# Kernel optimization log

Measured on AMD Instinct MI355X. Metric: run time of the kernel, lower is better.

Reference implementation:

```python
import jax, jax.numpy as jnp
import numpy as np

N = 50000
E = 800000
IN_FEAT = 128
HEADS = 2
HEAD_DIM = 64  # hidden_feat // num_heads for 'concat'
HIDDEN = HEADS * HEAD_DIM
N_CLASSES = 16
NEG_SLOPE = 0.2
BN_EPS = 1e-5


def setup_inputs() -> dict:
    key = jax.random.key(0)
    ks = jax.random.split(key, 20)
    s = 0.1  # weight scale for numerical sanity
    return {
        "x": jax.random.normal(ks[0], (N, IN_FEAT), jnp.float32),
        "src0": jax.random.randint(ks[1], (E,), 0, N, jnp.int32),
        "dst0": jax.random.randint(ks[2], (E,), 0, N, jnp.int32),
        "ew0": jax.random.uniform(ks[3], (E,), jnp.float32),
        "src1": jax.random.randint(ks[4], (E,), 0, N, jnp.int32),
        "dst1": jax.random.randint(ks[5], (E,), 0, N, jnp.int32),
        "ew1": jax.random.uniform(ks[6], (E,), jnp.float32),
        "fc_w0": jax.random.normal(ks[7], (HIDDEN, IN_FEAT), jnp.float32) * s,
        "bias0": jnp.zeros((HIDDEN,), jnp.float32),
        "attn_l0": jax.random.normal(ks[8], (HEADS, HEAD_DIM), jnp.float32) * s,
        "attn_r0": jax.random.normal(ks[9], (HEADS, HEAD_DIM), jnp.float32) * s,
        "fc_w1": jax.random.normal(ks[10], (HIDDEN, IN_FEAT), jnp.float32) * s,
        "bias1": jnp.zeros((HIDDEN,), jnp.float32),
        "attn_l1": jax.random.normal(ks[11], (HEADS, HEAD_DIM), jnp.float32) * s,
        "attn_r1": jax.random.normal(ks[12], (HEADS, HEAD_DIM), jnp.float32) * s,
        "skip_w": jax.random.normal(ks[13], (HIDDEN, IN_FEAT), jnp.float32) * s,
        "skip_b": jnp.zeros((HIDDEN,), jnp.float32),
        "bn_gamma": jnp.ones((HIDDEN,), jnp.float32),
        "bn_beta": jnp.zeros((HIDDEN,), jnp.float32),
        "clf_w": jax.random.normal(ks[14], (N_CLASSES, HIDDEN), jnp.float32) * s,
        "clf_b": jnp.zeros((N_CLASSES,), jnp.float32),
    }


def _weighted_gat(x, src, dst, ew, fc_w, bias, attn_l, attn_r):
    # DGL GATConv with per-edge weight scaling of attention.
    f = (x @ fc_w.T).reshape(N, HEADS, HEAD_DIM)          # [N,H,D]
    el = jnp.sum(f * attn_l, axis=-1)                      # [N,H]
    er = jnp.sum(f * attn_r, axis=-1)                      # [N,H]
    e = jax.nn.leaky_relu(el[src] + er[dst], NEG_SLOPE)    # [E,H]
    # edge softmax over incoming edges of each dst, numerically stable
    m = jax.ops.segment_max(e, dst, num_segments=N)        # [N,H]
    ex = jnp.exp(e - m[dst])
    den = jax.ops.segment_sum(ex, dst, num_segments=N)     # [N,H]
    alpha = ex / den[dst]                                  # [E,H]
    alpha = alpha * ew[:, None]                            # edge-weight scaling
    msg = alpha[..., None] * f[src]                        # [E,H,D]
    out = jax.ops.segment_sum(msg, dst, num_segments=N)    # [N,H,D]
    return out + bias.reshape(1, HEADS, HEAD_DIM)


def reference(x, src0, dst0, ew0, src1, dst1, ew1,
              fc_w0, bias0, attn_l0, attn_r0,
              fc_w1, bias1, attn_l1, attn_r1,
              skip_w, skip_b, bn_gamma, bn_beta, clf_w, clf_b):
    # HeteroGraphConv with aggregate='sum': sum per-relation GAT outputs
    h2 = _weighted_gat(x, src0, dst0, ew0, fc_w0, bias0, attn_l0, attn_r0) \
       + _weighted_gat(x, src1, dst1, ew1, fc_w1, bias1, attn_l1, attn_r1)
    # multihead 'concat' aggregate with relu: flatten heads
    h2 = jax.nn.relu(h2).reshape(N, HIDDEN)
    # linear skip + residual add (dropout is identity at eval)
    h = (x @ skip_w.T + skip_b) + h2
    # classifier: BatchNorm1d (batch stats) -> ReLU -> Linear
    mu = jnp.mean(h, axis=0)
    var = jnp.mean((h - mu) ** 2, axis=0)
    hn = (h - mu) * jax.lax.rsqrt(var + BN_EPS) * bn_gamma + bn_beta
    logits = jax.nn.relu(hn) @ clf_w.T + clf_b
    return logits
```

## Files before the change

kernel.cpp:

```cpp
#include <hip/hip_runtime.h>
#include <hip/hip_bf16.h>

#define N_NODES 50000
#define N_EDGES 800000
#define HID 128
#define NEG_SLOPE 0.2f
#define BN_EPS 1e-5f

#define NBLK 256
#define BINSZ 512
#define BINSH 9
#define NBINS 98

typedef __bf16 v8bf __attribute__((ext_vector_type(8)));
typedef float v4f __attribute__((ext_vector_type(4)));

__device__ __forceinline__ float leaky(float v) {
    return (v > 0.f) ? v : v * NEG_SLOPE;
}
__device__ __forceinline__ unsigned int f2bu(float f) {
    __hip_bfloat16 b = __float2bfloat16(f);
    return (unsigned int)*reinterpret_cast<unsigned short*>(&b);
}
__device__ __forceinline__ unsigned int pack2bf(float lo, float hi) {
    return f2bu(lo) | (f2bu(hi) << 16);
}

__global__ __launch_bounds__(256) void k_bincount(const int* __restrict__ dst0,
                                                  const int* __restrict__ dst1,
                                                  int* __restrict__ bincnt) {
    int rel = blockIdx.y;
    const int* dst = rel ? dst1 : dst0;
    __shared__ int cnt[NBINS];
    for (int i = threadIdx.x; i < NBINS; i += 256) cnt[i] = 0;
    __syncthreads();
    const int CH = (N_EDGES + NBLK - 1) / NBLK;
    int b0 = blockIdx.x * CH;
    int b1 = min(N_EDGES, b0 + CH);
    for (int e = b0 + threadIdx.x; e < b1; e += 256)
        atomicAdd(&cnt[dst[e] >> BINSH], 1);
    __syncthreads();
    for (int i = threadIdx.x; i < NBINS; i += 256)
        bincnt[rel * NBINS * NBLK + i * NBLK + blockIdx.x] = cnt[i];
}

__global__ __launch_bounds__(1024) void k_binscan(int* __restrict__ bincnt) {
    int* a = bincnt + blockIdx.x * NBINS * NBLK;
    const int TOT = NBINS * NBLK;
    const int CH = (TOT + 1023) / 1024;
    int tid = threadIdx.x;
    int base = tid * CH;
    int lv[CH];
    int sum = 0;
    for (int i = 0; i < CH; i++) {
        int idx = base + i;
        int v = (idx < TOT) ? a[idx] : 0;
        lv[i] = sum;
        sum += v;
    }
    __shared__ int ls[1024];
    ls[tid] = sum;
    __syncthreads();
    for (int ofs = 1; ofs < 1024; ofs <<= 1) {
        int v = (tid >= ofs) ? ls[tid - ofs] : 0;
        __syncthreads();
        ls[tid] += v;
        __syncthreads();
    }
    int pre = tid ? ls[tid - 1] : 0;
    for (int i = 0; i < CH; i++) {
        int idx = base + i;
        if (idx < TOT) a[idx] = pre + lv[i];
    }
}

__global__ __launch_bounds__(256) void k_binscatter(const int* __restrict__ dst0,
                                                    const int* __restrict__ dst1,
                                                    const int* __restrict__ src0,
                                                    const int* __restrict__ src1,
                                                    const float* __restrict__ ew0,
                                                    const float* __restrict__ ew1,
                                                    const int* __restrict__ bincnt,
                                                    int2* __restrict__ pairs0,
                                                    int2* __restrict__ pairs1) {
    int rel = blockIdx.y;
    const int* dst = rel ? dst1 : dst0;
    const int* src = rel ? src1 : src0;
    const float* ew = rel ? ew1 : ew0;
    int2* pairs = rel ? pairs1 : pairs0;
    __shared__ int cur[NBINS];
    for (int i = threadIdx.x; i < NBINS; i += 256)
        cur[i] = bincnt[rel * NBINS * NBLK + i * NBLK + blockIdx.x];
    __syncthreads();
    const int CH = (N_EDGES + NBLK - 1) / NBLK;
    int b0 = blockIdx.x * CH;
    int b1 = min(N_EDGES, b0 + CH);
    for (int e = b0 + threadIdx.x; e < b1; e += 256) {
        int d = dst[e];
        int pos = atomicAdd(&cur[d >> BINSH], 1);
        unsigned int packed = (unsigned int)(d & (BINSZ - 1)) |
                              ((unsigned int)src[e] << BINSH);
        pairs[pos] = make_int2((int)packed, __float_as_int(ew[e]));
    }
}

__global__ __launch_bounds__(256) void k_csr(const int* __restrict__ bincnt,
                                             const int2* __restrict__ pairs0,
                                             const int2* __restrict__ pairs1,
                                             const float* __restrict__ el0,
                                             const float* __restrict__ el1,
                                             int* __restrict__ offs0,
                                             int* __restrict__ offs1,
                                             int4* __restrict__ rec0,
                                             int4* __restrict__ rec1) {
    int rel = blockIdx.y;
    const int2* pairs = rel ? pairs1 : pairs0;
    const float* el = rel ? el1 : el0;
    int* offs = rel ? offs1 : offs0;
    int4* rec = rel ? rec1 : rec0;
    int bin = blockIdx.x;
    int tid = threadIdx.x;
    const int* bc = bincnt + rel * NBINS * NBLK;
    int pbase = bc[bin * NBLK];
    int pend = (bin < NBINS - 1) ? bc[(bin + 1) * NBLK] : N_EDGES;
    int n0 = bin << BINSH;
    int nn = min(N_NODES - n0, BINSZ);

    __shared__ int s_deg[BINSZ];
    __shared__ int s_ts[256];
    for (int i = tid; i < BINSZ; i += 256) s_deg[i] = 0;
    __syncthreads();
    for (int p = pbase + tid; p < pend; p += 256)
        atomicAdd(&s_deg[((unsigned int)pairs[p].x) & (BINSZ - 1)], 1);
    __syncthreads();

    int d0 = s_deg[tid * 2], d1 = s_deg[tid * 2 + 1];
    s_ts[tid] = d0 + d1;
    __syncthreads();
    for (int ofs = 1; ofs < 256; ofs <<= 1) {
        int v = (tid >= ofs) ? s_ts[tid - ofs] : 0;
        __syncthreads();
        s_ts[tid] += v;
        __syncthreads();
    }
    int pre = tid ? s_ts[tid - 1] : 0;
    s_deg[tid * 2] = pbase + pre;
    s_deg[tid * 2 + 1] = pbase + pre + d0;
    __syncthreads();

    for (int l = tid; l < nn; l += 256) offs[n0 + l] = s_deg[l];
    if (bin == NBINS - 1 && tid == 0) offs[N_NODES] = N_EDGES;
    __syncthreads();

    for (int p = pbase + tid; p < pend; p += 256) {
        int2 pr = pairs[p];
        unsigned int u = (unsigned int)pr.x;
        int dl = (int)(u & (BINSZ - 1));
        int s = (int)(u >> BINSH);
        int pos = atomicAdd(&s_deg[dl], 1);
        float2 ev = *(const float2*)(el + 2 * s);
        rec[pos] = make_int4(s, pr.y,
                             __float_as_int(ev.x), __float_as_int(ev.y));
    }
}

__global__ __launch_bounds__(256) void k_gemm_mfma(
    const float* __restrict__ x,
    const float* __restrict__ w0, const float* __restrict__ w1,
    const float* __restrict__ wsk, const float* __restrict__ skip_b,
    const float* __restrict__ al0, const float* __restrict__ ar0,
    const float* __restrict__ al1, const float* __restrict__ ar1,
    unsigned short* __restrict__ fb0, unsigned short* __restrict__ fb1,
    float* __restrict__ el0, float* __restrict__ er0,
    float* __restrict__ el1, float* __restrict__ er1,
    float* __restrict__ hs) {
    __shared__ unsigned short As[64][128];
    __shared__ unsigned short Bs[64][128];
    int tid = threadIdx.x;
    int m0 = blockIdx.x * 64;

#pragma unroll
    for (int i = 0; i < 4; i++) {
        int idx = tid * 4 + i;
        int row = idx >> 4, seg = idx & 15;
        int gr = m0 + row;
        uint4 o = make_uint4(0, 0, 0, 0);
        if (gr < N_NODES) {
            const float* p = x + (size_t)gr * HID + seg * 8;
            float4 p0 = *(const float4*)p;
            float4 p1 = *(const float4*)(p + 4);
            o.x = pack2bf(p0.x, p0.y);
            o.y = pack2bf(p0.z, p0.w);
            o.z = pack2bf(p1.x, p1.y);
            o.w = pack2bf(p1.z, p1.w);
        }
        *(uint4*)(&As[row][(seg ^ (row & 7)) * 8]) = o;
    }
    __syncthreads();

    int w = tid >> 6, l = tid & 63;
    int lr = l & 15, lg = l >> 4;
    int arow = w * 16 + lr;
    v8bf afrag[4];
#pragma unroll
    for (int kb = 0; kb < 4; kb++)
        afrag[kb] = *(v8bf*)(&As[arow][((kb * 4 + lg) ^ (arow & 7)) * 8]);

    for (int s = 0; s < 6; s++) {
        int mat = s >> 1;
        int j0 = (s & 1) * 64;
        const float* W = (mat == 0) ? w0 : (mat == 1) ? w1 : wsk;
        __syncthreads();
#pragma unroll
        for (int i = 0; i < 4; i++) {
            int idx = tid * 4 + i;
            int row = idx >> 4, seg = idx & 15;
            const float* p = W + (size_t)(j0 + row) * HID + seg * 8;
            float4 p0 = *(const float4*)p;
            float4 p1 = *(const float4*)(p + 4);
            uint4 o;
            o.x = pack2bf(p0.x, p0.y);
            o.y = pack2bf(p0.z, p0.w);
            o.z = pack2bf(p1.x, p1.y);
            o.w = pack2bf(p1.z, p1.w);
            *(uint4*)(&Bs[row][(seg ^ (row & 7)) * 8]) = o;
        }
        __syncthreads();

        v4f acc[4] = {};
#pragma unroll
        for (int nt = 0; nt < 4; nt++) {
            int brow = nt * 16 + lr;
#pragma unroll
            for (int kb = 0; kb < 4; kb++) {
                v8bf bfrag =
                    *(v8bf*)(&Bs[brow][((kb * 4 + lg) ^ (brow & 7)) * 8]);
                acc[nt] = __builtin_amdgcn_mfma_f32_16x16x32_bf16(
                    afrag[kb], bfrag, acc[nt], 0, 0, 0);
            }
        }

        if (mat < 2) {
            int h = s & 1;
            const float* al = mat ? al1 : al0;
            const float* ar = mat ? ar1 : ar0;
            float* elp = mat ? el1 : el0;
            float* erp = mat ? er1 : er0;
            unsigned short* fbp = mat ? fb1 : fb0;
            float elv[4] = {0.f, 0.f, 0.f, 0.f};
            float erv[4] = {0.f, 0.f, 0.f, 0.f};
#pragma unroll
            for (int nt = 0; nt < 4; nt++) {
                int colg = j0 + nt * 16 + lr;
                float av = al[colg], rv = ar[colg];
#pragma unroll
                for (int r = 0; r < 4; r++) {
                    elv[r] += acc[nt][r] * av;
                    erv[r] += acc[nt][r] * rv;
                }
            }
#pragma unroll
            for (int m = 1; m < 16; m <<= 1)
#pragma unroll
                for (int r = 0; r < 4; r++) {
                    elv[r] += __shfl_xor(elv[r], m);
                    erv[r] += __shfl_xor(erv[r], m);
                }
#pragma unroll
            for (int r = 0; r < 4; r++) {
                int grow = m0 + w * 16 + lg * 4 + r;
                if (grow >= N_NODES) continue;
#pragma unroll
                for (int nt = 0; nt < 4; nt++) {
                    int colg = j0 + nt * 16 + lr;
                    fbp[(size_t)grow * HID + colg] =
                        (unsigned short)f2bu(acc[nt][r]);
                }
                if (lr == 0) {
                    elp[grow * 2 + h] = elv[r];
                    erp[grow * 2 + h] = erv[r];
                }
            }
        } else {
#pragma unroll
            for (int r = 0; r < 4; r++) {
                int grow = m0 + w * 16 + lg * 4 + r;
                if (grow >= N_NODES) continue;
#pragma unroll
                for (int nt = 0; nt < 4; nt++) {
                    int colg = j0 + nt * 16 + lr;
                    hs[(size_t)grow * HID + colg] = acc[nt][r] + skip_b[colg];
                }
            }
        }
    }
}

__device__ __forceinline__ void agg_rel2(const int* __restrict__ offs,
                                         const int4* __restrict__ rec,
                                         const float* __restrict__ er,
                                         const unsigned short* __restrict__ fb,
                                         int n, int lane, int cb, int sub,
                                         int hh, float* a) {
    int b = offs[n];
    int e_end = offs[n + 1];
    int deg = e_end - b;
    if (deg <= 0) return;
    float ern0 = er[2 * n], ern1 = er[2 * n + 1];

    const int NC = 4;
    int cs[NC];
    float cw0[NC], cw1[NC];
    unsigned int cpk[NC];
    float d0 = 0.f, d1 = 0.f;
    int nchunk = (deg + 63) >> 6;
    for (int ch = 0; ch < nchunk; ch++) {
        int p = b + (ch << 6) + lane;
        int s = 0;
        float w0 = 0.f, w1 = 0.f;
        if (p < e_end) {
            int4 r = rec[p];
            s = r.x;
            float wgt = __int_as_float(r.y);
            float x0 = expf(leaky(__int_as_float(r.z) + ern0));
            float x1 = expf(leaky(__int_as_float(r.w) + ern1));
            d0 += x0;
            d1 += x1;
            w0 = x0 * wgt;
            w1 = x1 * wgt;
        }
        if (ch < NC) {
            cs[ch] = s;
            cw0[ch] = w0;
            cw1[ch] = w1;
        }
    }
#pragma unroll
    for (int m = 32; m; m >>= 1) {
        d0 += __shfl_xor(d0, m);
        d1 += __shfl_xor(d1, m);
    }
    float inv0 = 1.f / d0, inv1 = 1.f / d1;
#pragma unroll
    for (int ch = 0; ch < NC; ch++)
        cpk[ch] = pack2bf(cw0[ch] * inv0, cw1[ch] * inv1);

    for (int ch = 0; ch < nchunk; ch++) {
        int s;
        unsigned int pk;
        if (ch < NC) {
            s = cs[ch];
            pk = cpk[ch];
        } else {
            int p = b + (ch << 6) + lane;
            s = 0;
            pk = 0;
            if (p < e_end) {
                int4 r = rec[p];
                s = r.x;
                float wgt = __int_as_float(r.y);
                float w0 = expf(leaky(__int_as_float(r.z) + ern0)) * wgt;
                float w1 = expf(leaky(__int_as_float(r.w) + ern1)) * wgt;
                pk = pack2bf(w0 * inv0, w1 * inv1);
            }
        }
        int cnt = deg - (ch << 6);
        if (cnt > 64) cnt = 64;
        int ng = (cnt + 3) >> 2;
#pragma unroll 2
        for (int g = 0; g < ng; g++) {
            int sl = (g << 2) + sub;
            int sj = __shfl(s, sl);
            unsigned int pkj = (unsigned int)__shfl((int)pk, sl);
            float aj = __uint_as_float(hh ? (pkj & 0xffff0000u) : (pkj << 16));
            uint4 fv = *(const uint4*)(fb + (size_t)sj * HID + cb * 8);
            a[0] += aj * __uint_as_float(fv.x << 16);
            a[1] += aj * __uint_as_float(fv.x & 0xffff0000u);
            a[2] += aj * __uint_as_float(fv.y << 16);
            a[3] += aj * __uint_as_float(fv.y & 0xffff0000u);
            a[4] += aj * __uint_as_float(fv.z << 16);
            a[5] += aj * __uint_as_float(fv.z & 0xffff0000u);
            a[6] += aj * __uint_as_float(fv.w << 16);
            a[7] += aj * __uint_as_float(fv.w & 0xffff0000u);
        }
    }
}

__global__ __launch_bounds__(256) void k_aggregate(
    const int* __restrict__ offs0, const int4* __restrict__ rec0,
    const float* __restrict__ er0, const unsigned short* __restrict__ fb0,
    const int* __restrict__ offs1, const int4* __restrict__ rec1,
    const float* __restrict__ er1, const unsigned short* __restrict__ fb1,
    const float* __restrict__ bias0, const float* __restrict__ bias1,
    float* __restrict__ h) {
    int wave = threadIdx.x >> 6, lane = threadIdx.x & 63;
    int n = blockIdx.x * 4 + wave;
    if (n >= N_NODES) return;
    int cb = lane & 15;
    int sub = lane >> 4;
    int hh = cb >> 3;
    float a[8] = {0.f, 0.f, 0.f, 0.f, 0.f, 0.f, 0.f, 0.f};
    agg_rel2(offs0, rec0, er0, fb0, n, lane, cb, sub, hh, a);
    agg_rel2(offs1, rec1, er1, fb1, n, lane, cb, sub, hh, a);
#pragma unroll
    for (int j = 0; j < 8; j++) {
        a[j] += __shfl_xor(a[j], 16);
        a[j] += __shfl_xor(a[j], 32);
    }
    if (sub == 0) {
        size_t base = (size_t)n * HID + cb * 8;
        float4 v0 = *(const float4*)(h + base);
        float4 v1 = *(const float4*)(h + base + 4);
        int c0 = cb * 8;
        float4 o0, o1;
        o0.x = v0.x + fmaxf(a[0] + bias0[c0 + 0] + bias1[c0 + 0], 0.f);
        o0.y = v0.y + fmaxf(a[1] + bias0[c0 + 1] + bias1[c0 + 1], 0.f);
        o0.z = v0.z + fmaxf(a[2] + bias0[c0 + 2] + bias1[c0 + 2], 0.f);
        o0.w = v0.w + fmaxf(a[3] + bias0[c0 + 3] + bias1[c0 + 3], 0.f);
        o1.x = v1.x + fmaxf(a[4] + bias0[c0 + 4] + bias1[c0 + 4], 0.f);
        o1.y = v1.y + fmaxf(a[5] + bias0[c0 + 5] + bias1[c0 + 5], 0.f);
        o1.z = v1.z + fmaxf(a[6] + bias0[c0 + 6] + bias1[c0 + 6], 0.f);
        o1.w = v1.w + fmaxf(a[7] + bias0[c0 + 7] + bias1[c0 + 7], 0.f);
        *(float4*)(h + base) = o0;
        *(float4*)(h + base + 4) = o1;
    }
}

__global__ __launch_bounds__(256) void k_bnstats(const float* __restrict__ h,
                                                 double* __restrict__ psum,
                                                 double* __restrict__ psumsq) {
    int tid = threadIdx.x;
    double s = 0.0, q = 0.0;
    const int total = N_NODES * HID;
    const int stride = 512 * 256;
    for (int idx = blockIdx.x * 256 + tid; idx < total; idx += stride) {
        float v = h[idx];
        s += v;
        q += (double)v * v;
    }
    __shared__ double ls[256], lq[256];
    ls[tid] = s;
    lq[tid] = q;
    __syncthreads();
    if (tid < 128) {
        psum[blockIdx.x * 128 + tid] = ls[tid] + ls[tid + 128];
        psumsq[blockIdx.x * 128 + tid] = lq[tid] + lq[tid + 128];
    }
}

__global__ void k_bn_finalize(const double* __restrict__ psum,
                              const double* __restrict__ psumsq,
                              const float* __restrict__ gamma,
                              const float* __restrict__ beta,
                              float* __restrict__ ss) {
    int c = threadIdx.x;
    double s = 0.0, q = 0.0;
    for (int b = 0; b < 512; b++) {
        s += psum[b * 128 + c];
        q += psumsq[b * 128 + c];
    }
    double mu = s / N_NODES;
    double var = q / N_NODES - mu * mu;
    float sc = gamma[c] * (float)(1.0 / sqrt(var + (double)BN_EPS));
    ss[c] = sc;
    ss[128 + c] = beta[c] - (float)mu * sc;
}

__global__ __launch_bounds__(256) void k_classify(const float* __restrict__ h,
                                                  const float* __restrict__ ss,
                                                  const float* __restrict__ clf_w,
                                                  const float* __restrict__ clf_b,
                                                  float* __restrict__ out) {
    int w = threadIdx.x >> 6, l = threadIdx.x & 63;
    int lr = l & 15, lg = l >> 4;
    int n0 = (blockIdx.x * 4 + w) * 16;
    if (n0 >= N_NODES) return;

    v8bf afrag[4], bfrag[4];
#pragma unroll
    for (int kb = 0; kb < 4; kb++) {
        int k0 = kb * 32 + lg * 8;
        const float* bp = clf_w + lr * HID + k0;
        float4 b0 = *(const float4*)bp;
        float4 b1 = *(const float4*)(bp + 4);
        bfrag[kb][0] = (__bf16)b0.x; bfrag[kb][1] = (__bf16)b0.y;
        bfrag[kb][2] = (__bf16)b0.z; bfrag[kb][3] = (__bf16)b0.w;
        bfrag[kb][4] = (__bf16)b1.x; bfrag[kb][5] = (__bf16)b1.y;
        bfrag[kb][6] = (__bf16)b1.z; bfrag[kb][7] = (__bf16)b1.w;
        const float* ap = h + (size_t)(n0 + lr) * HID + k0;
        float4 a0 = *(const float4*)ap;
        float4 a1 = *(const float4*)(ap + 4);
        float4 sc0 = *(const float4*)(ss + k0);
        float4 sc1 = *(const float4*)(ss + k0 + 4);
        float4 sh0 = *(const float4*)(ss + 128 + k0);
        float4 sh1 = *(const float4*)(ss + 128 + k0 + 4);
        afrag[kb][0] = (__bf16)fmaxf(a0.x * sc0.x + sh0.x, 0.f);
        afrag[kb][1] = (__bf16)fmaxf(a0.y * sc0.y + sh0.y, 0.f);
        afrag[kb][2] = (__bf16)fmaxf(a0.z * sc0.z + sh0.z, 0.f);
        afrag[kb][3] = (__bf16)fmaxf(a0.w * sc0.w + sh0.w, 0.f);
        afrag[kb][4] = (__bf16)fmaxf(a1.x * sc1.x + sh1.x, 0.f);
        afrag[kb][5] = (__bf16)fmaxf(a1.y * sc1.y + sh1.y, 0.f);
        afrag[kb][6] = (__bf16)fmaxf(a1.z * sc1.z + sh1.z, 0.f);
        afrag[kb][7] = (__bf16)fmaxf(a1.w * sc1.w + sh1.w, 0.f);
    }
    v4f acc = {};
#pragma unroll
    for (int kb = 0; kb < 4; kb++)
        acc = __builtin_amdgcn_mfma_f32_16x16x32_bf16(afrag[kb], bfrag[kb],
                                                      acc, 0, 0, 0);
    float cb = clf_b[lr];
#pragma unroll
    for (int r = 0; r < 4; r++) {
        int n = n0 + lg * 4 + r;
        out[(size_t)n * 16 + lr] = acc[r] + cb;
    }
}

extern "C" void kernel_launch(void* const* d_in, const int* in_sizes, int n_in,
                              void* d_out, int out_size, void* d_ws, size_t ws_size,
                              hipStream_t stream) {
    (void)in_sizes; (void)n_in; (void)out_size; (void)ws_size;
    const float* x      = (const float*)d_in[0];
    const int*   src0   = (const int*)d_in[1];
    const int*   dst0   = (const int*)d_in[2];
    const float* ew0    = (const float*)d_in[3];
    const int*   src1   = (const int*)d_in[4];
    const int*   dst1   = (const int*)d_in[5];
    const float* ew1    = (const float*)d_in[6];
    const float* fc_w0  = (const float*)d_in[7];
    const float* bias0  = (const float*)d_in[8];
    const float* al0    = (const float*)d_in[9];
    const float* ar0    = (const float*)d_in[10];
    const float* fc_w1  = (const float*)d_in[11];
    const float* bias1  = (const float*)d_in[12];
    const float* al1    = (const float*)d_in[13];
    const float* ar1    = (const float*)d_in[14];
    const float* skip_w = (const float*)d_in[15];
    const float* skip_b = (const float*)d_in[16];
    const float* gamma  = (const float*)d_in[17];
    const float* beta   = (const float*)d_in[18];
    const float* clf_w  = (const float*)d_in[19];
    const float* clf_b  = (const float*)d_in[20];
    float* out = (float*)d_out;

    char* wsp = (char*)d_ws;
    size_t off = 0;
    auto alloc = [&](size_t bytes) -> char* {
        char* p = wsp + off;
        off += (bytes + 255) & ~(size_t)255;
        return p;
    };
    unsigned short* fb0 = (unsigned short*)alloc((size_t)N_NODES * HID * 2);
    unsigned short* fb1 = (unsigned short*)alloc((size_t)N_NODES * HID * 2);
    float*  hs     = (float*)alloc((size_t)N_NODES * HID * 4);
    float*  el0    = (float*)alloc((size_t)N_NODES * 2 * 4);
    float*  er0    = (float*)alloc((size_t)N_NODES * 2 * 4);
    float*  el1    = (float*)alloc((size_t)N_NODES * 2 * 4);
    float*  er1    = (float*)alloc((size_t)N_NODES * 2 * 4);
    int*    bincnt = (int*)alloc((size_t)2 * NBINS * NBLK * 4);
    int2*   pairs0 = (int2*)alloc((size_t)N_EDGES * 8);
    int2*   pairs1 = (int2*)alloc((size_t)N_EDGES * 8);
    int*    offs0  = (int*)alloc((size_t)(N_NODES + 1) * 4);
    int*    offs1  = (int*)alloc((size_t)(N_NODES + 1) * 4);
    int4*   rec0   = (int4*)alloc((size_t)N_EDGES * 16);
    int4*   rec1   = (int4*)alloc((size_t)N_EDGES * 16);
    double* psum   = (double*)alloc((size_t)512 * 128 * 8);
    double* psumsq = (double*)alloc((size_t)512 * 128 * 8);
    float*  ss     = (float*)alloc(256 * 4);

    dim3 gbin(NBLK, 2);
    k_bincount<<<gbin, 256, 0, stream>>>(dst0, dst1, bincnt);
    k_binscan<<<2, 1024, 0, stream>>>(bincnt);
    k_binscatter<<<gbin, 256, 0, stream>>>(dst0, dst1, src0, src1, ew0, ew1,
                                           bincnt, pairs0, pairs1);

    k_gemm_mfma<<<(N_NODES + 63) / 64, 256, 0, stream>>>(
        x, fc_w0, fc_w1, skip_w, skip_b, al0, ar0, al1, ar1,
        fb0, fb1, el0, er0, el1, er1, hs);

    dim3 gcsr(NBINS, 2);
    k_csr<<<gcsr, 256, 0, stream>>>(bincnt, pairs0, pairs1, el0, el1,
                                    offs0, offs1, rec0, rec1);

    k_aggregate<<<(N_NODES + 3) / 4, 256, 0, stream>>>(
        offs0, rec0, er0, fb0, offs1, rec1, er1, fb1, bias0, bias1, hs);

    k_bnstats<<<512, 256, 0, stream>>>(hs, psum, psumsq);
    k_bn_finalize<<<1, 128, 0, stream>>>(psum, psumsq, gamma, beta, ss);
    k_classify<<<(N_NODES + 15) / 16 / 4 + 1, 256, 0, stream>>>(
        hs, ss, clf_w, clf_b, out);
}
```

Before: 235.3 us.

## Pre-convert weights to bf16, stage edge data in LDS, vectorize BN stats

A new kernel converts the three weight matrices to bf16 once, so the GEMM reads B fragments straight from global memory instead of converting and staging them through shared memory with two barriers per step. In aggregation, per-edge source index and packed weights go through a per-wave LDS buffer rather than two shuffles per edge, and the unroll depth is raised. The BN statistics kernel now reads float4s and reduces per channel in shared memory. Risks are unswizzled, uncoalesced global B loads, an extra launch, and the classify grid size changing.

```diff
diff --git a/kernel.cpp b/kernel.cpp
--- a/kernel.cpp
+++ b/kernel.cpp
@@ -24,6 +24,25 @@
 }
 __device__ __forceinline__ unsigned int pack2bf(float lo, float hi) {
     return f2bu(lo) | (f2bu(hi) << 16);
+}
+
+__global__ __launch_bounds__(256) void k_prepw(const float* __restrict__ w0,
+                                               const float* __restrict__ w1,
+                                               const float* __restrict__ wsk,
+                                               unsigned short* __restrict__ wb) {
+    const int WQ = 128 * 128 / 4;
+    int q = blockIdx.x * 256 + threadIdx.x;
+    if (q >= 3 * WQ) return;
+    int mat = q >> 12;
+    int rem = q & 4095;
+    const float* W = (mat == 0) ? w0 : (mat == 1) ? w1 : wsk;
+    float4 v = ((const float4*)W)[rem];
+    ushort4 o;
+    o.x = (unsigned short)f2bu(v.x);
+    o.y = (unsigned short)f2bu(v.y);
+    o.z = (unsigned short)f2bu(v.z);
+    o.w = (unsigned short)f2bu(v.w);
+    *(ushort4*)(wb + (size_t)mat * 16384 + rem * 4) = o;
 }
 
 __global__ __launch_bounds__(256) void k_bincount(const int* __restrict__ dst0,
@@ -165,9 +184,8 @@
 }
 
 __global__ __launch_bounds__(256) void k_gemm_mfma(
-    const float* __restrict__ x,
-    const float* __restrict__ w0, const float* __restrict__ w1,
-    const float* __restrict__ wsk, const float* __restrict__ skip_b,
+    const float* __restrict__ x, const unsigned short* __restrict__ wb,
+    const float* __restrict__ skip_b,
     const float* __restrict__ al0, const float* __restrict__ ar0,
     const float* __restrict__ al1, const float* __restrict__ ar1,
     unsigned short* __restrict__ fb0, unsigned short* __restrict__ fb1,
@@ -175,7 +193,6 @@
     float* __restrict__ el1, float* __restrict__ er1,
     float* __restrict__ hs) {
     __shared__ unsigned short As[64][128];
-    __shared__ unsigned short Bs[64][128];
     int tid = threadIdx.x;
     int m0 = blockIdx.x * 64;
 
@@ -209,32 +226,15 @@
     for (int s = 0; s < 6; s++) {
         int mat = s >> 1;
         int j0 = (s & 1) * 64;
-        const float* W = (mat == 0) ? w0 : (mat == 1) ? w1 : wsk;
-        __syncthreads();
-#pragma unroll
-        for (int i = 0; i < 4; i++) {
-            int idx = tid * 4 + i;
-            int row = idx >> 4, seg = idx & 15;
-            const float* p = W + (size_t)(j0 + row) * HID + seg * 8;
-            float4 p0 = *(const float4*)p;
-            float4 p1 = *(const float4*)(p + 4);
-            uint4 o;
-            o.x = pack2bf(p0.x, p0.y);
-            o.y = pack2bf(p0.z, p0.w);
-            o.z = pack2bf(p1.x, p1.y);
-            o.w = pack2bf(p1.z, p1.w);
-            *(uint4*)(&Bs[row][(seg ^ (row & 7)) * 8]) = o;
-        }
-        __syncthreads();
+        const unsigned short* wmat = wb + (size_t)mat * 16384;
 
         v4f acc[4] = {};
 #pragma unroll
         for (int nt = 0; nt < 4; nt++) {
-            int brow = nt * 16 + lr;
+            const unsigned short* brow = wmat + (size_t)(j0 + nt * 16 + lr) * HID;
 #pragma unroll
             for (int kb = 0; kb < 4; kb++) {
-                v8bf bfrag =
-                    *(v8bf*)(&Bs[brow][((kb * 4 + lg) ^ (brow & 7)) * 8]);
+                v8bf bfrag = *(const v8bf*)(brow + kb * 32 + lg * 8);
                 acc[nt] = __builtin_amdgcn_mfma_f32_16x16x32_bf16(
                     afrag[kb], bfrag, acc[nt], 0, 0, 0);
             }
@@ -296,12 +296,13 @@
     }
 }
 
-__device__ __forceinline__ void agg_rel2(const int* __restrict__ offs,
+__device__ __forceinline__ void agg_rel3(const int* __restrict__ offs,
                                          const int4* __restrict__ rec,
                                          const float* __restrict__ er,
                                          const unsigned short* __restrict__ fb,
                                          int n, int lane, int cb, int sub,
-                                         int hh, float* a) {
+                                         int hh, float* a,
+                                         unsigned long long* __restrict__ sed) {
     int b = offs[n];
     int e_end = offs[n + 1];
     int deg = e_end - b;
@@ -311,7 +312,6 @@
     const int NC = 4;
     int cs[NC];
     float cw0[NC], cw1[NC];
-    unsigned int cpk[NC];
     float d0 = 0.f, d1 = 0.f;
     int nchunk = (deg + 63) >> 6;
     for (int ch = 0; ch < nchunk; ch++) {
@@ -341,16 +341,14 @@
         d1 += __shfl_xor(d1, m);
     }
     float inv0 = 1.f / d0, inv1 = 1.f / d1;
-#pragma unroll
-    for (int ch = 0; ch < NC; ch++)
-        cpk[ch] = pack2bf(cw0[ch] * inv0, cw1[ch] * inv1);
+    const unsigned short* fbc = fb + cb * 8;
 
     for (int ch = 0; ch < nchunk; ch++) {
         int s;
         unsigned int pk;
         if (ch < NC) {
             s = cs[ch];
-            pk = cpk[ch];
+            pk = pack2bf(cw0[ch] * inv0, cw1[ch] * inv1);
         } else {
             int p = b + (ch << 6) + lane;
             s = 0;
@@ -359,21 +357,22 @@
                 int4 r = rec[p];
                 s = r.x;
                 float wgt = __int_as_float(r.y);
-                float w0 = expf(leaky(__int_as_float(r.z) + ern0)) * wgt;
-                float w1 = expf(leaky(__int_as_float(r.w) + ern1)) * wgt;
-                pk = pack2bf(w0 * inv0, w1 * inv1);
+                pk = pack2bf(expf(leaky(__int_as_float(r.z) + ern0)) * wgt * inv0,
+                             expf(leaky(__int_as_float(r.w) + ern1)) * wgt * inv1);
             }
         }
+        sed[lane] = ((unsigned long long)pk << 32) | (unsigned int)s;
+        asm volatile("s_waitcnt lgkmcnt(0)" ::: "memory");
         int cnt = deg - (ch << 6);
         if (cnt > 64) cnt = 64;
         int ng = (cnt + 3) >> 2;
-#pragma unroll 2
+#pragma unroll 4
         for (int g = 0; g < ng; g++) {
-            int sl = (g << 2) + sub;
-            int sj = __shfl(s, sl);
-            unsigned int pkj = (unsigned int)__shfl((int)pk, sl);
+            unsigned long long v = sed[(g << 2) + sub];
+            int sj = (int)(unsigned int)v;
+            unsigned int pkj = (unsigned int)(v >> 32);
             float aj = __uint_as_float(hh ? (pkj & 0xffff0000u) : (pkj << 16));
-            uint4 fv = *(const uint4*)(fb + (size_t)sj * HID + cb * 8);
+            uint4 fv = *(const uint4*)(fbc + (size_t)sj * HID);
             a[0] += aj * __uint_as_float(fv.x << 16);
             a[1] += aj * __uint_as_float(fv.x & 0xffff0000u);
             a[2] += aj * __uint_as_float(fv.y << 16);
@@ -393,6 +392,7 @@
     const float* __restrict__ er1, const unsigned short* __restrict__ fb1,
     const float* __restrict__ bias0, const float* __restrict__ bias1,
     float* __restrict__ h) {
+    __shared__ unsigned long long sed[4][64];
     int wave = threadIdx.x >> 6, lane = threadIdx.x & 63;
     int n = blockIdx.x * 4 + wave;
     if (n >= N_NODES) return;
@@ -400,8 +400,8 @@
     int sub = lane >> 4;
     int hh = cb >> 3;
     float a[8] = {0.f, 0.f, 0.f, 0.f, 0.f, 0.f, 0.f, 0.f};
-    agg_rel2(offs0, rec0, er0, fb0, n, lane, cb, sub, hh, a);
-    agg_rel2(offs1, rec1, er1, fb1, n, lane, cb, sub, hh, a);
+    agg_rel3(offs0, rec0, er0, fb0, n, lane, cb, sub, hh, a, &sed[wave][0]);
+    agg_rel3(offs1, rec1, er1, fb1, n, lane, cb, sub, hh, a, &sed[wave][0]);
 #pragma unroll
     for (int j = 0; j < 8; j++) {
         a[j] += __shfl_xor(a[j], 16);
@@ -430,21 +430,36 @@
                                                  double* __restrict__ psum,
                                                  double* __restrict__ psumsq) {
     int tid = threadIdx.x;
-    double s = 0.0, q = 0.0;
-    const int total = N_NODES * HID;
+    const float4* h4 = (const float4*)h;
+    double s[4] = {0.0, 0.0, 0.0, 0.0};
+    double q[4] = {0.0, 0.0, 0.0, 0.0};
+    const int totalv = N_NODES * HID / 4;
     const int stride = 512 * 256;
-    for (int idx = blockIdx.x * 256 + tid; idx < total; idx += stride) {
-        float v = h[idx];
-        s += v;
-        q += (double)v * v;
-    }
-    __shared__ double ls[256], lq[256];
-    ls[tid] = s;
-    lq[tid] = q;
-    __syncthreads();
-    if (tid < 128) {
-        psum[blockIdx.x * 128 + tid] = ls[tid] + ls[tid + 128];
-        psumsq[blockIdx.x * 128 + tid] = lq[tid] + lq[tid + 128];
+    for (int i = blockIdx.x * 256 + tid; i < totalv; i += stride) {
+        float4 v = h4[i];
+        s[0] += v.x; q[0] += (double)v.x * v.x;
+        s[1] += v.y; q[1] += (double)v.y * v.y;
+        s[2] += v.z; q[2] += (double)v.z * v.z;
+        s[3] += v.w; q[3] += (double)v.w * v.w;
+    }
+    __shared__ double ls[256][4], lq[256][4];
+#pragma unroll
+    for (int j = 0; j < 4; j++) {
+        ls[tid][j] = s[j];
+        lq[tid][j] = q[j];
+    }
+    __syncthreads();
+    if (tid < 32) {
+#pragma unroll
+        for (int j = 0; j < 4; j++) {
+            double ss = 0.0, qq = 0.0;
+            for (int t = tid; t < 256; t += 32) {
+                ss += ls[t][j];
+                qq += lq[t][j];
+            }
+            psum[blockIdx.x * 128 + tid * 4 + j] = ss;
+            psumsq[blockIdx.x * 128 + tid * 4 + j] = qq;
+        }
     }
 }
 
@@ -550,6 +565,7 @@
         off += (bytes + 255) & ~(size_t)255;
         return p;
     };
+    unsigned short* wbf = (unsigned short*)alloc((size_t)3 * 16384 * 2);
     unsigned short* fb0 = (unsigned short*)alloc((size_t)N_NODES * HID * 2);
     unsigned short* fb1 = (unsigned short*)alloc((size_t)N_NODES * HID * 2);
     float*  hs     = (float*)alloc((size_t)N_NODES * HID * 4);
@@ -568,6 +584,8 @@
     double* psumsq = (double*)alloc((size_t)512 * 128 * 8);
     float*  ss     = (float*)alloc(256 * 4);
 
+    k_prepw<<<48, 256, 0, stream>>>(fc_w0, fc_w1, skip_w, wbf);
+
     dim3 gbin(NBLK, 2);
     k_bincount<<<gbin, 256, 0, stream>>>(dst0, dst1, bincnt);
     k_binscan<<<2, 1024, 0, stream>>>(bincnt);
@@ -575,7 +593,7 @@
                                            bincnt, pairs0, pairs1);
 
     k_gemm_mfma<<<(N_NODES + 63) / 64, 256, 0, stream>>>(
-        x, fc_w0, fc_w1, skip_w, skip_b, al0, ar0, al1, ar1,
+        x, wbf, skip_b, al0, ar0, al1, ar1,
         fb0, fb1, el0, er0, el1, er1, hs);
 
     dim3 gcsr(NBINS, 2);
@@ -587,6 +605,6 @@
 
     k_bnstats<<<512, 256, 0, stream>>>(hs, psum, psumsq);
     k_bn_finalize<<<1, 128, 0, stream>>>(psum, psumsq, gamma, beta, ss);
-    k_classify<<<(N_NODES + 15) / 16 / 4 + 1, 256, 0, stream>>>(
+    k_classify<<<(N_NODES + 63) / 64, 256, 0, stream>>>(
         hs, ss, clf_w, clf_b, out);
 }
```

Measured after the change: 259.4 us. +10.2%, slower.
